# Optimization experiments

Hardware: AMD Instinct MI355X
Metric: run time of the kernel (lower is better)

## Reference

```python
import jax, jax.numpy as jnp
import numpy as np

WIN = 8      # win_size
HEADS = 8    # num_heads


def setup_inputs() -> dict:
    key = jax.random.key(0)
    k0, k1, k2 = jax.random.split(key, 3)
    b, H, W, C = 8, 256, 256, 64
    seq = WIN * WIN
    x = jax.random.normal(k0, (b, H, W, C), jnp.float32)
    W_qkv = jax.random.normal(k1, (3 * C, C), jnp.float32) * 0.05  # 1x1 point-conv weight
    b_qkv = jnp.zeros((3 * C,), jnp.float32)
    # trunc_normal_(std=1, a=-2, b=2) approximated by clipped normal
    pos_emb = jnp.clip(jax.random.normal(k2, (1, HEADS, seq, seq), jnp.float32), -2.0, 2.0)
    return {"x": x, "W_qkv": W_qkv, "b_qkv": b_qkv, "pos_emb": pos_emb}


def reference(x, W_qkv, b_qkv, pos_emb):
    b, H, W, C = x.shape
    heads, win = HEADS, WIN
    hc = C // heads
    seq = win * win
    nh, nw = H // win, W // win
    m = nh * nw  # number of windows
    # 'b (h i) (w j) c -> b m (i j) c' windowing
    xw = x.reshape(b, nh, win, nw, win, C).transpose(0, 1, 3, 2, 4, 5).reshape(b, m, seq, C)
    # 1x1 conv over channels == per-position linear
    qkv = jnp.einsum('bmnc,dc->bmnd', xw, W_qkv) + b_qkv  # [b, m, seq, 3C]
    q, k, v = jnp.split(qkv, 3, axis=-1)
    # '(h c)' channel order is heads-major, matching rearrange 'b (h c) m n -> (b m) h n c'
    def split_heads(t):
        return t.reshape(b, m, seq, heads, hc).transpose(0, 1, 3, 2, 4)  # [b, m, h, seq, hc]
    q, k, v = map(split_heads, (q, k, v))
    scale = hc ** (-0.5)
    sim = jnp.einsum('bmhic,bmhjc->bmhij', q * scale, k) + pos_emb[0]  # bias bcast over b, m
    attn = jax.nn.softmax(sim, axis=-1)
    out = jnp.einsum('bmhij,bmhjc->bmhic', attn, v)  # [b, m, h, seq, hc]
    # 'b h n c -> (b m) n (h c)'
    out = out.transpose(0, 1, 3, 2, 4).reshape(b * m, seq, C)
    return out
```

## Files before the change

### kernel.cpp

```cpp
#include <hip/hip_runtime.h>
#include <math.h>


typedef __attribute__((ext_vector_type(8)))  short bf16x8;
typedef __attribute__((ext_vector_type(4)))  float f32x4;
typedef __attribute__((ext_vector_type(16))) float f32x16;

__device__ inline unsigned int cvt_pk_bf16(float lo, float hi) {
    unsigned int r;
    asm("v_cvt_pk_bf16_f32 %0, %1, %2" : "=v"(r) : "v"(lo), "v"(hi));
    return r;
}
__device__ inline unsigned short f2bf(float f) {
    unsigned int u = __builtin_bit_cast(unsigned int, f);
    return (unsigned short)((u + 0x7FFFu + ((u >> 16) & 1u)) >> 16);
}
#define BFLO(u) __builtin_bit_cast(float, (unsigned int)((u) << 16))
#define BFHI(u) __builtin_bit_cast(float, (unsigned int)((u) & 0xffff0000u))

__device__ inline bf16x8 pack8(float4 a, float4 b) {
    union { unsigned int u[4]; bf16x8 v; } r;
    r.u[0] = cvt_pk_bf16(a.x, a.y);
    r.u[1] = cvt_pk_bf16(a.z, a.w);
    r.u[2] = cvt_pk_bf16(b.x, b.y);
    r.u[3] = cvt_pk_bf16(b.z, b.w);
    return r.v;
}

__global__ __launch_bounds__(256) void prep_pos(const float* __restrict__ pos,
                                                unsigned short* __restrict__ pp)
{
    int flat = blockIdx.x * 256 + threadIdx.x;
    int r  = flat & 15;
    int ln = (flat >> 4) & 63;
    int jt = (flat >> 10) & 1;
    int it = (flat >> 11) & 1;
    int h  = flat >> 12;
    int j = jt*32 + (r & 3) + 8*(r >> 2) + 4*(ln >> 5);
    int i = it*32 + (ln & 31);
    pp[flat] = f2bf(pos[(h*64 + i)*64 + j] * 1.4426950408889634f);
}

__global__ __launch_bounds__(256, 3) void lm_mfma(const float* __restrict__ x,
                                                  const float* __restrict__ Wq,
                                                  const float* __restrict__ bq,
                                                  const unsigned short* __restrict__ pp,
                                                  float* __restrict__ out)
{
    __shared__ unsigned short sPool[4*32*64];
    __shared__ unsigned short sQ [64*64];
    __shared__ unsigned short sK [64*64];
    __shared__ unsigned short sVT[64*64];
    unsigned short* const sX = sPool;
    unsigned short* const sP = sPool;

    const int tid = threadIdx.x;
    const int w   = blockIdx.x;
    const int ln  = tid & 63;
    const int wv  = tid >> 6;
    const int lr  = ln & 15;
    const int lg  = ln >> 4;

    const int bi = w >> 10, mm = w & 1023;
    const int mh = mm >> 5, mw = mm & 31;
    const float* xwin = x + ((size_t)(bi*256 + mh*8)*256 + mw*8)*64;

    #pragma unroll
    for (int r = 0; r < 4; ++r) {
        const int f4 = tid + r*256;
        const int n  = f4 >> 4;
        const int c  = (f4 & 15) * 4;
        const float4 v = *(const float4*)(xwin + ((size_t)(n>>3)*256 + (n&7))*64 + c);
        uint2 u;
        u.x = cvt_pk_bf16(v.x, v.y);
        u.y = cvt_pk_bf16(v.z, v.w);
        *(uint2*)&sX[n*64 + (((c>>3) ^ (n&7))<<3) + (c&7)] = u;
    }

    bf16x8 wfrag[3][2];
    #pragma unroll
    for (int t = 0; t < 3; ++t) {
        const int d = (wv + 4*t)*16 + lr;
        #pragma unroll
        for (int kt = 0; kt < 2; ++kt) {
            const float* base = Wq + (size_t)d*64 + kt*32 + lg*8;
            wfrag[t][kt] = pack8(*(const float4*)base, *(const float4*)(base+4));
        }
    }
    const float qs = 0.35355339059327373f * 1.4426950408889634f;
    const float4 bqQr = *(const float4*)(bq       + wv*16 + lg*4);
    const float4 bqK  = *(const float4*)(bq + 64  + wv*16 + lg*4);
    const float  bqV  = bq[128 + wv*16 + lr];
    float4 bqQs;
    bqQs.x = bqQr.x*qs; bqQs.y = bqQr.y*qs; bqQs.z = bqQr.z*qs; bqQs.w = bqQr.w*qs;

    __syncthreads();

    f32x4 aQ[4], aK[4], aV[4];
    #pragma unroll
    for (int nt = 0; nt < 4; ++nt) { aQ[nt]=0; aK[nt]=0; aV[nt]=0; }

    #pragma unroll
    for (int nt = 0; nt < 4; ++nt) {
        #pragma unroll
        for (int kt = 0; kt < 2; ++kt) {
            const int n  = lr + nt*16;
            const int c8 = lg + kt*4;
            const bf16x8 xf = *(const bf16x8*)&sX[n*64 + ((c8 ^ (n&7))<<3)];
            aQ[nt] = __builtin_amdgcn_mfma_f32_16x16x32_bf16(wfrag[0][kt], xf, aQ[nt], 0,0,0);
            aK[nt] = __builtin_amdgcn_mfma_f32_16x16x32_bf16(wfrag[1][kt], xf, aK[nt], 0,0,0);
            aV[nt] = __builtin_amdgcn_mfma_f32_16x16x32_bf16(xf, wfrag[2][kt], aV[nt], 0,0,0);
        }
    }

    #pragma unroll
    for (int nt = 0; nt < 4; ++nt) {
        const int n  = lr + nt*16;
        const int d0 = wv*16 + lg*4;
        const int qidx = n*64 + (((d0>>3) ^ (n&7))<<3) + (d0&7);
        uint2 uq, uk;
        uq.x = cvt_pk_bf16(fmaf(aQ[nt][0], qs, bqQs.x), fmaf(aQ[nt][1], qs, bqQs.y));
        uq.y = cvt_pk_bf16(fmaf(aQ[nt][2], qs, bqQs.z), fmaf(aQ[nt][3], qs, bqQs.w));
        uk.x = cvt_pk_bf16(aK[nt][0]+bqK.x, aK[nt][1]+bqK.y);
        uk.y = cvt_pk_bf16(aK[nt][2]+bqK.z, aK[nt][3]+bqK.w);
        *(uint2*)&sQ[qidx] = uq;
        *(uint2*)&sK[qidx] = uk;
        const int cc = wv*16 + lr;
        const int n0 = nt*16 + lg*4;
        uint2 uv;
        uv.x = cvt_pk_bf16(aV[nt][0]+bqV, aV[nt][1]+bqV);
        uv.y = cvt_pk_bf16(aV[nt][2]+bqV, aV[nt][3]+bqV);
        *(uint2*)&sVT[cc*64 + (((n0>>3) ^ (cc&7))<<3) + (n0&7)] = uv;
    }

    __syncthreads();

    unsigned short* const pw = sP + ((wv*32 + (ln & 31)) << 6);
    const int il  = ln & 31;
    const int hi4 = (ln >> 5) * 4;

    #pragma unroll 1
    for (int hh = 0; hh < 2; ++hh) {
        const int h = wv*2 + hh;

        bf16x8 vf[2];
        #pragma unroll
        for (int kt = 0; kt < 2; ++kt) {
            bf16x8 z = {};
            vf[kt] = z;
            if (lr < 8) {
                const int cc = h*8 + lr;
                const int j0 = kt*32 + lg*8;
                vf[kt] = *(const bf16x8*)&sVT[cc*64 + (((j0>>3) ^ (cc&7))<<3)];
            }
        }

        f32x16 C[2][2];
        #pragma unroll
        for (int it = 0; it < 2; ++it)
            #pragma unroll
            for (int jt = 0; jt < 2; ++jt) {
                const unsigned short* pb = pp + (((h*2+it)*2 + jt)*64 + ln)*16;
                const uint4 a = *(const uint4*)(pb);
                const uint4 b = *(const uint4*)(pb + 8);
                C[it][jt][0]=BFLO(a.x);  C[it][jt][1]=BFHI(a.x);
                C[it][jt][2]=BFLO(a.y);  C[it][jt][3]=BFHI(a.y);
                C[it][jt][4]=BFLO(a.z);  C[it][jt][5]=BFHI(a.z);
                C[it][jt][6]=BFLO(a.w);  C[it][jt][7]=BFHI(a.w);
                C[it][jt][8]=BFLO(b.x);  C[it][jt][9]=BFHI(b.x);
                C[it][jt][10]=BFLO(b.y); C[it][jt][11]=BFHI(b.y);
                C[it][jt][12]=BFLO(b.z); C[it][jt][13]=BFHI(b.z);
                C[it][jt][14]=BFLO(b.w); C[it][jt][15]=BFHI(b.w);
            }

        bf16x8 qf0 = {}, qf1 = {}, kf0 = {}, kf1 = {};
        if (ln < 32) {
            qf0 = *(const bf16x8*)&sQ[ln*64 + ((h ^ (ln&7))<<3)];
            const int i1 = 32 + ln;
            qf1 = *(const bf16x8*)&sQ[i1*64 + ((h ^ (i1&7))<<3)];
            kf0 = *(const bf16x8*)&sK[ln*64 + ((h ^ (ln&7))<<3)];
            kf1 = *(const bf16x8*)&sK[i1*64 + ((h ^ (i1&7))<<3)];
        }
        C[0][0] = __builtin_amdgcn_mfma_f32_32x32x16_bf16(kf0, qf0, C[0][0], 0,0,0);
        C[0][1] = __builtin_amdgcn_mfma_f32_32x32x16_bf16(kf1, qf0, C[0][1], 0,0,0);
        C[1][0] = __builtin_amdgcn_mfma_f32_32x32x16_bf16(kf0, qf1, C[1][0], 0,0,0);
        C[1][1] = __builtin_amdgcn_mfma_f32_32x32x16_bf16(kf1, qf1, C[1][1], 0,0,0);

        f32x4 O[2][2];
        #pragma unroll
        for (int it = 0; it < 2; ++it) {
            float t[8];
            #pragma unroll
            for (int jt = 0; jt < 2; ++jt)
                #pragma unroll
                for (int g = 0; g < 4; ++g) {
                    const int b = g*4;
                    C[it][jt][b+0] = __builtin_amdgcn_exp2f(C[it][jt][b+0]);
                    C[it][jt][b+1] = __builtin_amdgcn_exp2f(C[it][jt][b+1]);
                    C[it][jt][b+2] = __builtin_amdgcn_exp2f(C[it][jt][b+2]);
                    C[it][jt][b+3] = __builtin_amdgcn_exp2f(C[it][jt][b+3]);
                    t[jt*4+g] = (C[it][jt][b+0]+C[it][jt][b+1])
                              + (C[it][jt][b+2]+C[it][jt][b+3]);
                }
            const float sum = ((t[0]+t[1])+(t[2]+t[3])) + ((t[4]+t[5])+(t[6]+t[7]));
            const float tot = sum + __shfl_xor(sum, 32, 64);
            const float iv  = __builtin_amdgcn_rcpf(tot);

            #pragma unroll
            for (int jt = 0; jt < 2; ++jt)
                #pragma unroll
                for (int G = 0; G < 4; ++G) {
                    uint2 u;
                    u.x = cvt_pk_bf16(C[it][jt][4*G+0]*iv, C[it][jt][4*G+1]*iv);
                    u.y = cvt_pk_bf16(C[it][jt][4*G+2]*iv, C[it][jt][4*G+3]*iv);
                    const int j0 = jt*32 + 8*G + hi4;
                    *(uint2*)&pw[(((j0>>3) ^ (il&7))<<3) + (j0&7)] = u;
                }

            O[it][0] = 0; O[it][1] = 0;
            #pragma unroll
            for (int pit = 0; pit < 2; ++pit)
                #pragma unroll
                for (int kt = 0; kt < 2; ++kt) {
                    const int i = pit*16 + lr;
                    const bf16x8 pf = *(const bf16x8*)&sP[(wv*32+i)*64
                                      + (((kt*4+lg) ^ (i&7))<<3)];
                    O[it][pit] = __builtin_amdgcn_mfma_f32_16x16x32_bf16(pf, vf[kt],
                                                                         O[it][pit], 0,0,0);
                }
        }

        if (lr < 8) {
            #pragma unroll
            for (int it = 0; it < 2; ++it)
                #pragma unroll
                for (int pit = 0; pit < 2; ++pit) {
                    float* ob = out + (size_t)w*4096
                              + (size_t)(it*32 + pit*16 + lg*4)*64 + h*8 + lr;
                    ob[0]   = O[it][pit][0];
                    ob[64]  = O[it][pit][1];
                    ob[128] = O[it][pit][2];
                    ob[192] = O[it][pit][3];
                }
        }
    }
}

extern "C" void kernel_launch(void* const* d_in, const int* in_sizes, int n_in,
                              void* d_out, int out_size, void* d_ws, size_t ws_size,
                              hipStream_t stream)
{
    const float* x   = (const float*)d_in[0];
    const float* Wq  = (const float*)d_in[1];
    const float* bq  = (const float*)d_in[2];
    const float* pos = (const float*)d_in[3];
    float* out = (float*)d_out;
    unsigned short* pp = (unsigned short*)d_ws;

    hipLaunchKernelGGL(prep_pos, dim3(128), dim3(256), 0, stream, pos, pp);
    hipLaunchKernelGGL(lm_mfma, dim3(8192), dim3(256), 0, stream, x, Wq, bq, pp, out);
}
```

Baseline: 98.77 us.

## Keep softmax probabilities in registers via permlane swap for PV MFMA

The softmax probabilities are no longer staged through shared memory between the QK^T and PV MFMAs. The exp results are packed to bf16 in registers, rearranged across lanes with v_permlane32_swap into B-operand layout, and fed to four 32x32x16 MFMAs computing V^T·P. Normalization by the row sum now happens after the PV product, and each lane writes a contiguous float4 instead of scalar stores. This removes the LDS write/read round trip and its memory traffic. It relies on the exact MFMA register layout being correct, and it rounds the unnormalized exponentials to bf16.

After: 99.72 us. No clear change (+1.0%).

```diff
diff --git a/kernel.cpp b/kernel.cpp
--- a/kernel.cpp
+++ b/kernel.cpp
@@ -10,6 +10,9 @@
     unsigned int r;
     asm("v_cvt_pk_bf16_f32 %0, %1, %2" : "=v"(r) : "v"(lo), "v"(hi));
     return r;
+}
+__device__ inline void permswap(unsigned int &a, unsigned int &b) {
+    asm("v_permlane32_swap_b32 %0, %1" : "+v"(a), "+v"(b));
 }
 __device__ inline unsigned short f2bf(float f) {
     unsigned int u = __builtin_bit_cast(unsigned int, f);
@@ -47,12 +50,10 @@
                                                   const unsigned short* __restrict__ pp,
                                                   float* __restrict__ out)
 {
-    __shared__ unsigned short sPool[4*32*64];
+    __shared__ unsigned short sX [64*64];
     __shared__ unsigned short sQ [64*64];
     __shared__ unsigned short sK [64*64];
     __shared__ unsigned short sVT[64*64];
-    unsigned short* const sX = sPool;
-    unsigned short* const sP = sPool;
 
     const int tid = threadIdx.x;
     const int w   = blockIdx.x;
@@ -135,23 +136,21 @@
 
     __syncthreads();
 
-    unsigned short* const pw = sP + ((wv*32 + (ln & 31)) << 6);
-    const int il  = ln & 31;
-    const int hi4 = (ln >> 5) * 4;
+    const int il = ln & 31;
+    const int hi = ln >> 5;
 
     #pragma unroll 1
     for (int hh = 0; hh < 2; ++hh) {
         const int h = wv*2 + hh;
 
-        bf16x8 vf[2];
-        #pragma unroll
-        for (int kt = 0; kt < 2; ++kt) {
+        bf16x8 vb[4];
+        #pragma unroll
+        for (int q = 0; q < 4; ++q) {
             bf16x8 z = {};
-            vf[kt] = z;
-            if (lr < 8) {
-                const int cc = h*8 + lr;
-                const int j0 = kt*32 + lg*8;
-                vf[kt] = *(const bf16x8*)&sVT[cc*64 + (((j0>>3) ^ (cc&7))<<3)];
+            vb[q] = z;
+            if (il < 8) {
+                const int cc = h*8 + il;
+                vb[q] = *(const bf16x8*)&sVT[cc*64 + (((2*q+hi) ^ (cc&7))<<3)];
             }
         }
 
@@ -186,19 +185,39 @@
         C[1][0] = __builtin_amdgcn_mfma_f32_32x32x16_bf16(kf0, qf1, C[1][0], 0,0,0);
         C[1][1] = __builtin_amdgcn_mfma_f32_32x32x16_bf16(kf1, qf1, C[1][1], 0,0,0);
 
-        f32x4 O[2][2];
         #pragma unroll
         for (int it = 0; it < 2; ++it) {
+            #pragma unroll
+            for (int jt = 0; jt < 2; ++jt)
+                #pragma unroll
+                for (int e = 0; e < 16; ++e)
+                    C[it][jt][e] = __builtin_amdgcn_exp2f(C[it][jt][e]);
+
+            union { unsigned int u[4]; bf16x8 v; } B[4];
+            #pragma unroll
+            for (int jt = 0; jt < 2; ++jt) {
+                unsigned int a0 = cvt_pk_bf16(C[it][jt][0],  C[it][jt][1]);
+                unsigned int a1 = cvt_pk_bf16(C[it][jt][2],  C[it][jt][3]);
+                unsigned int a2 = cvt_pk_bf16(C[it][jt][4],  C[it][jt][5]);
+                unsigned int a3 = cvt_pk_bf16(C[it][jt][6],  C[it][jt][7]);
+                unsigned int a4 = cvt_pk_bf16(C[it][jt][8],  C[it][jt][9]);
+                unsigned int a5 = cvt_pk_bf16(C[it][jt][10], C[it][jt][11]);
+                unsigned int a6 = cvt_pk_bf16(C[it][jt][12], C[it][jt][13]);
+                unsigned int a7 = cvt_pk_bf16(C[it][jt][14], C[it][jt][15]);
+                permswap(a0, a2);  permswap(a1, a3);
+                permswap(a4, a6);  permswap(a5, a7);
+                B[2*jt].u[0]   = a0; B[2*jt].u[1]   = a1;
+                B[2*jt].u[2]   = a2; B[2*jt].u[3]   = a3;
+                B[2*jt+1].u[0] = a4; B[2*jt+1].u[1] = a5;
+                B[2*jt+1].u[2] = a6; B[2*jt+1].u[3] = a7;
+            }
+
             float t[8];
             #pragma unroll
             for (int jt = 0; jt < 2; ++jt)
                 #pragma unroll
                 for (int g = 0; g < 4; ++g) {
                     const int b = g*4;
-                    C[it][jt][b+0] = __builtin_amdgcn_exp2f(C[it][jt][b+0]);
-                    C[it][jt][b+1] = __builtin_amdgcn_exp2f(C[it][jt][b+1]);
-                    C[it][jt][b+2] = __builtin_amdgcn_exp2f(C[it][jt][b+2]);
-                    C[it][jt][b+3] = __builtin_amdgcn_exp2f(C[it][jt][b+3]);
                     t[jt*4+g] = (C[it][jt][b+0]+C[it][jt][b+1])
                               + (C[it][jt][b+2]+C[it][jt][b+3]);
                 }
@@ -206,42 +225,19 @@
             const float tot = sum + __shfl_xor(sum, 32, 64);
             const float iv  = __builtin_amdgcn_rcpf(tot);
 
-            #pragma unroll
-            for (int jt = 0; jt < 2; ++jt)
-                #pragma unroll
-                for (int G = 0; G < 4; ++G) {
-                    uint2 u;
-                    u.x = cvt_pk_bf16(C[it][jt][4*G+0]*iv, C[it][jt][4*G+1]*iv);
-                    u.y = cvt_pk_bf16(C[it][jt][4*G+2]*iv, C[it][jt][4*G+3]*iv);
-                    const int j0 = jt*32 + 8*G + hi4;
-                    *(uint2*)&pw[(((j0>>3) ^ (il&7))<<3) + (j0&7)] = u;
-                }
-
-            O[it][0] = 0; O[it][1] = 0;
-            #pragma unroll
-            for (int pit = 0; pit < 2; ++pit)
-                #pragma unroll
-                for (int kt = 0; kt < 2; ++kt) {
-                    const int i = pit*16 + lr;
-                    const bf16x8 pf = *(const bf16x8*)&sP[(wv*32+i)*64
-                                      + (((kt*4+lg) ^ (i&7))<<3)];
-                    O[it][pit] = __builtin_amdgcn_mfma_f32_16x16x32_bf16(pf, vf[kt],
-                                                                         O[it][pit], 0,0,0);
-                }
-        }
-
-        if (lr < 8) {
-            #pragma unroll
-            for (int it = 0; it < 2; ++it)
-                #pragma unroll
-                for (int pit = 0; pit < 2; ++pit) {
-                    float* ob = out + (size_t)w*4096
-                              + (size_t)(it*32 + pit*16 + lg*4)*64 + h*8 + lr;
-                    ob[0]   = O[it][pit][0];
-                    ob[64]  = O[it][pit][1];
-                    ob[128] = O[it][pit][2];
-                    ob[192] = O[it][pit][3];
-                }
+            f32x16 O = {};
+            O = __builtin_amdgcn_mfma_f32_32x32x16_bf16(vb[0], B[0].v, O, 0,0,0);
+            O = __builtin_amdgcn_mfma_f32_32x32x16_bf16(vb[1], B[1].v, O, 0,0,0);
+            O = __builtin_amdgcn_mfma_f32_32x32x16_bf16(vb[2], B[2].v, O, 0,0,0);
+            O = __builtin_amdgcn_mfma_f32_32x32x16_bf16(vb[3], B[3].v, O, 0,0,0);
+
+            float4 o;
+            o.x = O[0] * iv;
+            o.y = O[1] * iv;
+            o.z = O[2] * iv;
+            o.w = O[3] * iv;
+            *(float4*)(out + (size_t)w*4096 + (size_t)(it*32 + il)*64
+                       + h*8 + 4*hi) = o;
         }
     }
 }
```
